# Kernel optimization log

Hardware: AMD Instinct MI355X
Metric: run time of the kernel (lower is better)

Reference implementation:

```python
import jax, jax.numpy as jnp
import numpy as np
import math

D_MODEL = 512
N_HEADS = 8
PATH_LEN = 3
B, L, S = 4, 1024, 1024


def _path_index_structure(L, S, path_length):
    """Precompute the static multi-hop index structure (numpy, trace-time)."""
    i = np.arange(L)[:, None]          # [L,1]
    j = np.arange(S)[None, :]          # [1,S]
    step = (j - i) / path_length       # float
    # Python int() truncates toward zero; i + k*step >= 0 here, so floor == int().
    m1 = np.floor(i + 1 * step).astype(np.int32)  # [L,S] first intermediate point
    m2 = np.floor(i + 2 * step).astype(np.int32)  # [L,S] second intermediate point
    near = np.abs(i - j) <= path_length            # [L,S] bool: direct-score region
    return m1, m2, near


def setup_inputs() -> dict:
    key = jax.random.key(0)
    ks = jax.random.split(key, 7)
    inp = {
        "queries": jax.random.normal(ks[0], (B, L, D_MODEL), dtype=jnp.float32),
        "keys": jax.random.normal(ks[1], (B, S, D_MODEL), dtype=jnp.float32),
        "values": jax.random.normal(ks[2], (B, S, D_MODEL), dtype=jnp.float32),
        # nn.Linear(d_model, d_keys*n_heads, bias=False): stored as [in, out] so y = x @ W
        "W_q": jax.random.normal(ks[3], (D_MODEL, D_MODEL), dtype=jnp.float32) * 0.02,
        "W_k": jax.random.normal(ks[4], (D_MODEL, D_MODEL), dtype=jnp.float32) * 0.02,
        "W_v": jax.random.normal(ks[5], (D_MODEL, D_MODEL), dtype=jnp.float32) * 0.02,
        "W_o": jax.random.normal(ks[6], (D_MODEL, D_MODEL), dtype=jnp.float32) * 0.02,
    }
    return inp


def reference(queries, keys, values, W_q, W_k, W_v, W_o):
    Bv, Lv, _ = queries.shape
    Sv = keys.shape[1]
    H = N_HEADS
    q = (queries @ W_q).reshape(Bv, Lv, H, -1).transpose(0, 2, 1, 3)  # [B,H,L,D]
    k = (keys @ W_k).reshape(Bv, Sv, H, -1).transpose(0, 2, 1, 3)     # [B,H,S,D]
    v = (values @ W_v).reshape(Bv, Sv, H, -1).transpose(0, 2, 1, 3)   # [B,H,S,D]
    D = q.shape[-1]

    scores = jnp.einsum('bhld,bhsd->bhls', q, k) / math.sqrt(D)  # [B,H,L,S]

    # --- path-score modification (vectorized form of the nested loops) ---
    m1, m2, near = _path_index_structure(Lv, Sv, PATH_LEN)
    row = np.arange(Lv)[:, None]
    col = np.arange(Sv)[None, :]
    a = scores[:, :, row, m1]   # scores[:,:,i,m1(i,j)] -> [B,H,L,S]
    b = scores[:, :, m2, col]   # scores[:,:,m2(i,j),j] -> [B,H,L,S]
    # .mean() in the original reduces over BOTH batch and heads to a scalar per (i,j)
    path_mean = jnp.mean(a * b, axis=(0, 1))  # [L,S]
    scores = jnp.where(jnp.asarray(near), scores, path_mean[None, None, :, :])

    attn = jax.nn.softmax(scores, axis=-1)  # dropout p=0 in eval reference
    out = jnp.einsum('bhls,bhsd->blhd', attn, v).reshape(Bv, Lv, H * D)
    out = out @ W_o  # [B,L,d_model]
    return out, attn
```

## Files before the change

### kernel.cpp

```cpp
#include <hip/hip_runtime.h>
#include <math.h>

static constexpr int B_ = 4;
static constexpr int L_ = 1024;
static constexpr int S_ = 1024;
static constexpr int DMODEL = 512;
static constexpr int NH = 8;
static constexpr int DH = 64;
static constexpr int NBH = 32;

typedef __attribute__((ext_vector_type(8))) short s8;
typedef __attribute__((ext_vector_type(4))) float floatx4;

__device__ __forceinline__ short f2bf(float f) {
  unsigned u = __float_as_uint(f);
  return (short)((u + 0x7fffu + ((u >> 16) & 1u)) >> 16);
}
__device__ __forceinline__ float bf2f(short s) {
  return __uint_as_float(((unsigned)(unsigned short)s) << 16);
}

__global__ __launch_bounds__(256)
void cvt_inputs_kernel(const float* __restrict__ q, const float* __restrict__ k,
                       const float* __restrict__ v, short* __restrict__ dst) {
  const int i = blockIdx.x * 256 + threadIdx.x;
  const int arr = i >> 18;
  const int off = (i & 262143) << 3;
  const float* src = (arr == 0) ? q : (arr == 1) ? k : v;
  const float4 f0 = *(const float4*)(src + off);
  const float4 f1 = *(const float4*)(src + off + 4);
  s8 o;
  o[0] = f2bf(f0.x); o[1] = f2bf(f0.y); o[2] = f2bf(f0.z); o[3] = f2bf(f0.w);
  o[4] = f2bf(f1.x); o[5] = f2bf(f1.y); o[6] = f2bf(f1.z); o[7] = f2bf(f1.w);
  *(s8*)(dst + (size_t)arr * 2097152 + off) = o;
}

__global__ __launch_bounds__(256)
void wtrans_kernel(const float* __restrict__ Wq, const float* __restrict__ Wk,
                   const float* __restrict__ Wv, const float* __restrict__ Wo,
                   short* __restrict__ WT) {
  __shared__ float t[32][33];
  const int z = blockIdx.z;
  const float* W = (z == 0) ? Wq : (z == 1) ? Wk : (z == 2) ? Wv : Wo;
  short* dst = WT + (size_t)z * 262144;
  const int k0 = blockIdx.y * 32, n0 = blockIdx.x * 32;
  const int row = threadIdx.x >> 3;
  const int c4 = (threadIdx.x & 7) << 2;
  const float4 f = *(const float4*)(W + (size_t)(k0 + row) * 512 + n0 + c4);
  t[row][c4 + 0] = f.x; t[row][c4 + 1] = f.y; t[row][c4 + 2] = f.z; t[row][c4 + 3] = f.w;
  __syncthreads();
#pragma unroll
  for (int j = 0; j < 4; ++j)
    dst[(size_t)(n0 + row) * 512 + k0 + c4 + j] = f2bf(t[c4 + j][row]);
}

template<int MODE>
__global__ __launch_bounds__(256)
void proj_mfma_kernel(const short* __restrict__ A, const short* __restrict__ WT,
                      void* __restrict__ C, int K) {
  const int tid = threadIdx.x;
  const int lane = tid & 63, w = tid >> 6;
  const int wm = w >> 1, wn = w & 1;
  const int m0 = blockIdx.y * 64, n0 = blockIdx.x * 64;
  const int kl = (lane >> 4) << 3;
  const int rA = m0 + wm * 32 + (lane & 15);
  const int rB = n0 + wn * 32 + (lane & 15);
  const short* pA = A + (size_t)rA * K + kl;
  const short* pB = WT + (size_t)rB * K + kl;
  const size_t f16K = (size_t)16 * K;
  floatx4 acc00 = {0,0,0,0}, acc01 = {0,0,0,0}, acc10 = {0,0,0,0}, acc11 = {0,0,0,0};
  for (int k = 0; k < K; k += 32) {
    const s8 a0 = *(const s8*)(pA + k);
    const s8 a1 = *(const s8*)(pA + f16K + k);
    const s8 b0 = *(const s8*)(pB + k);
    const s8 b1 = *(const s8*)(pB + f16K + k);
    acc00 = __builtin_amdgcn_mfma_f32_16x16x32_bf16(a0, b0, acc00, 0, 0, 0);
    acc01 = __builtin_amdgcn_mfma_f32_16x16x32_bf16(a0, b1, acc01, 0, 0, 0);
    acc10 = __builtin_amdgcn_mfma_f32_16x16x32_bf16(a1, b0, acc10, 0, 0, 0);
    acc11 = __builtin_amdgcn_mfma_f32_16x16x32_bf16(a1, b1, acc11, 0, 0, 0);
  }
  const int crow = (lane >> 4) << 2;
  const int ccol = lane & 15;
#pragma unroll
  for (int fm = 0; fm < 2; ++fm)
#pragma unroll
    for (int fn = 0; fn < 2; ++fn) {
      const floatx4 acc = (fm == 0) ? ((fn == 0) ? acc00 : acc01)
                                    : ((fn == 0) ? acc10 : acc11);
      const int col = n0 + wn * 32 + fn * 16 + ccol;
#pragma unroll
      for (int r = 0; r < 4; ++r) {
        const int row = m0 + wm * 32 + fm * 16 + crow + r;
        if (MODE == 0) {
          const int b = row >> 10, l = row & 1023, h = col >> 6, d = col & 63;
          ((short*)C)[((size_t)((b * NH + h) * L_ + l)) * DH + d] = f2bf(acc[r]);
        } else if (MODE == 1) {
          const int b = row >> 10, s = row & 1023, h = col >> 6, d = col & 63;
          ((short*)C)[((size_t)((b * NH + h) * DH + d)) * S_ + s] = f2bf(acc[r]);
        } else {
          ((float*)C)[(size_t)row * DMODEL + col] = acc[r];
        }
      }
    }
}

__global__ __launch_bounds__(256)
void scores_mfma_kernel(const short* __restrict__ qbf, const short* __restrict__ kbf,
                        float* __restrict__ Sc) {
  const int tid = threadIdx.x;
  const int lane = tid & 63, w = tid >> 6;
  const int wm = w >> 1, wn = w & 1;
  const int m0 = blockIdx.y * 64, n0 = blockIdx.x * 64;
  const int bh = blockIdx.z;
  const int kl = (lane >> 4) << 3;
  const short* pA = qbf + (size_t)bh * L_ * DH + (size_t)(m0 + wm * 32 + (lane & 15)) * DH + kl;
  const short* pB = kbf + (size_t)bh * S_ * DH + (size_t)(n0 + wn * 32 + (lane & 15)) * DH + kl;
  floatx4 acc00 = {0,0,0,0}, acc01 = {0,0,0,0}, acc10 = {0,0,0,0}, acc11 = {0,0,0,0};
#pragma unroll
  for (int k = 0; k < DH; k += 32) {
    const s8 a0 = *(const s8*)(pA + k);
    const s8 a1 = *(const s8*)(pA + 16 * DH + k);
    const s8 b0 = *(const s8*)(pB + k);
    const s8 b1 = *(const s8*)(pB + 16 * DH + k);
    acc00 = __builtin_amdgcn_mfma_f32_16x16x32_bf16(a0, b0, acc00, 0, 0, 0);
    acc01 = __builtin_amdgcn_mfma_f32_16x16x32_bf16(a0, b1, acc01, 0, 0, 0);
    acc10 = __builtin_amdgcn_mfma_f32_16x16x32_bf16(a1, b0, acc10, 0, 0, 0);
    acc11 = __builtin_amdgcn_mfma_f32_16x16x32_bf16(a1, b1, acc11, 0, 0, 0);
  }
  float* Cp = Sc + (size_t)bh * L_ * S_;
  const int crow = (lane >> 4) << 2;
  const int ccol = lane & 15;
#pragma unroll
  for (int fm = 0; fm < 2; ++fm)
#pragma unroll
    for (int fn = 0; fn < 2; ++fn) {
      const floatx4 acc = (fm == 0) ? ((fn == 0) ? acc00 : acc01)
                                    : ((fn == 0) ? acc10 : acc11);
      const int col = n0 + wn * 32 + fn * 16 + ccol;
#pragma unroll
      for (int r = 0; r < 4; ++r) {
        const int row = m0 + wm * 32 + fm * 16 + crow + r;
        Cp[(size_t)row * S_ + col] = acc[r] * 0.125f;
      }
    }
}

__global__ __launch_bounds__(256)
void path_mean_kernel(const float* __restrict__ Sc, float* __restrict__ pm) {
  __shared__ float As[32][36];
  __shared__ float Bs[32][36];
  const int orig = blockIdx.x;
  const int wgid = (orig & 7) * 128 + (orig >> 3);
  const int i0 = (wgid >> 5) << 5;
  const int j0 = (wgid & 31) << 5;
  const int c0 = (2 * i0 + j0) / 3;
  const int c0_al = c0 & ~3;
  const int r0 = (i0 + 2 * j0) / 3;
  const int tid = threadIdx.x;
  const int row_s = tid >> 3;
  const int c4 = tid & 7;
  const int ti = tid >> 3;
  const int tj = tid & 7;
  const int gi = i0 + ti;
  int aoff[4], boff[4];
#pragma unroll
  for (int b = 0; b < 4; ++b) {
    const int gj = j0 + 4 * tj + b;
    const int m1 = (2 * gi + gj) / 3;
    const int m2 = (gi + 2 * gj) / 3;
    aoff[b] = ti * 36 + (m1 - c0_al);
    boff[b] = (m2 - r0) * 36 + (4 * tj + b);
  }
  const int gcA = c0_al + 4 * c4;
  int gcA2 = c0_al + 32; if (gcA2 > 1020) gcA2 = 1020;
  const float* pA  = Sc + (size_t)(i0 + row_s) * S_ + gcA;
  const float* pA2 = Sc + (size_t)(i0 + (tid & 31)) * S_ + gcA2;
  const float* pB  = Sc + (size_t)(r0 + row_s) * S_ + j0 + 4 * c4;
  const float* As0 = &As[0][0];
  const float* Bs0 = &Bs[0][0];
  float acc[4] = {0.f, 0.f, 0.f, 0.f};
  for (int z = 0; z < NBH; ++z) {
    const size_t zo = (size_t)z * (L_ * S_);
    const float4 av = *(const float4*)(pA + zo);
    const float4 bv = *(const float4*)(pB + zo);
    float4 av2;
    if (tid < 32) av2 = *(const float4*)(pA2 + zo);
    __syncthreads();
    *(float4*)&As[row_s][4 * c4] = av;
    if (tid < 32) *(float4*)&As[tid][32] = av2;
    *(float4*)&Bs[row_s][4 * c4] = bv;
    __syncthreads();
#pragma unroll
    for (int b = 0; b < 4; ++b)
      acc[b] = fmaf(As0[aoff[b]], Bs0[boff[b]], acc[b]);
  }
  float4 o = make_float4(acc[0] * (1.f / 32.f), acc[1] * (1.f / 32.f),
                         acc[2] * (1.f / 32.f), acc[3] * (1.f / 32.f));
  *(float4*)&pm[(size_t)gi * S_ + j0 + 4 * tj] = o;
}

__global__ __launch_bounds__(256)
void softmax_kernel(float* __restrict__ Sc, const float* __restrict__ pm) {
  const int r = blockIdx.x;
  const int i = r & 1023;
  float* row = Sc + (size_t)r * S_;
  const float* pmrow = pm + (size_t)i * S_;
  const int tid = threadIdx.x;
  const int j0 = tid << 2;
  const float4 sv = *(const float4*)(row + j0);
  const float4 pv = *(const float4*)(pmrow + j0);
  float vals[4] = {sv.x, sv.y, sv.z, sv.w};
  const float pvals[4] = {pv.x, pv.y, pv.z, pv.w};
  float mx = -1e30f;
#pragma unroll
  for (int u = 0; u < 4; ++u) {
    const int j = j0 + u;
    const int diff = i - j;
    const bool near = (diff <= 3) && (diff >= -3);
    vals[u] = near ? vals[u] : pvals[u];
    mx = fmaxf(mx, vals[u]);
  }
  __shared__ float redm[4];
  __shared__ float reds[4];
  const int lane = tid & 63, wid = tid >> 6;
#pragma unroll
  for (int off = 32; off >= 1; off >>= 1) mx = fmaxf(mx, __shfl_xor(mx, off));
  if (lane == 0) redm[wid] = mx;
  __syncthreads();
  mx = fmaxf(fmaxf(redm[0], redm[1]), fmaxf(redm[2], redm[3]));
  float sum = 0.f;
#pragma unroll
  for (int u = 0; u < 4; ++u) {
    vals[u] = __expf(vals[u] - mx);
    sum += vals[u];
  }
#pragma unroll
  for (int off = 32; off >= 1; off >>= 1) sum += __shfl_xor(sum, off);
  if (lane == 0) reds[wid] = sum;
  __syncthreads();
  sum = reds[0] + reds[1] + reds[2] + reds[3];
  const float inv = 1.f / sum;
  float4 o = make_float4(vals[0] * inv, vals[1] * inv, vals[2] * inv, vals[3] * inv);
  *(float4*)(row + j0) = o;
}

__global__ __launch_bounds__(256)
void pv_mfma_kernel(const float* __restrict__ attn, const short* __restrict__ vT,
                    short* __restrict__ out1) {
  const int tid = threadIdx.x;
  const int lane = tid & 63, w = tid >> 6;
  const int wm = w >> 1, wn = w & 1;
  const int m0 = blockIdx.x * 64;
  const int bh = blockIdx.y;
  const int b = bh >> 3, h = bh & 7;
  const int kl = (lane >> 4) << 3;
  const float* pA = attn + (size_t)bh * L_ * S_ + (size_t)(m0 + wm * 32 + (lane & 15)) * S_ + kl;
  const short* pB = vT + (size_t)bh * DH * S_ + (size_t)(wn * 32 + (lane & 15)) * S_ + kl;
  floatx4 acc00 = {0,0,0,0}, acc01 = {0,0,0,0}, acc10 = {0,0,0,0}, acc11 = {0,0,0,0};
  for (int k = 0; k < S_; k += 32) {
    const float4 fa0 = *(const float4*)(pA + k);
    const float4 fa1 = *(const float4*)(pA + k + 4);
    const float4 fb0 = *(const float4*)(pA + 16 * S_ + k);
    const float4 fb1 = *(const float4*)(pA + 16 * S_ + k + 4);
    s8 a0, a1;
    a0[0] = f2bf(fa0.x); a0[1] = f2bf(fa0.y); a0[2] = f2bf(fa0.z); a0[3] = f2bf(fa0.w);
    a0[4] = f2bf(fa1.x); a0[5] = f2bf(fa1.y); a0[6] = f2bf(fa1.z); a0[7] = f2bf(fa1.w);
    a1[0] = f2bf(fb0.x); a1[1] = f2bf(fb0.y); a1[2] = f2bf(fb0.z); a1[3] = f2bf(fb0.w);
    a1[4] = f2bf(fb1.x); a1[5] = f2bf(fb1.y); a1[6] = f2bf(fb1.z); a1[7] = f2bf(fb1.w);
    const s8 b0 = *(const s8*)(pB + k);
    const s8 b1 = *(const s8*)(pB + 16 * S_ + k);
    acc00 = __builtin_amdgcn_mfma_f32_16x16x32_bf16(a0, b0, acc00, 0, 0, 0);
    acc01 = __builtin_amdgcn_mfma_f32_16x16x32_bf16(a0, b1, acc01, 0, 0, 0);
    acc10 = __builtin_amdgcn_mfma_f32_16x16x32_bf16(a1, b0, acc10, 0, 0, 0);
    acc11 = __builtin_amdgcn_mfma_f32_16x16x32_bf16(a1, b1, acc11, 0, 0, 0);
  }
  const int crow = (lane >> 4) << 2;
  const int ccol = lane & 15;
#pragma unroll
  for (int fm = 0; fm < 2; ++fm)
#pragma unroll
    for (int fn = 0; fn < 2; ++fn) {
      const floatx4 acc = (fm == 0) ? ((fn == 0) ? acc00 : acc01)
                                    : ((fn == 0) ? acc10 : acc11);
      const int d = wn * 32 + fn * 16 + ccol;
#pragma unroll
      for (int r = 0; r < 4; ++r) {
        const int l = m0 + wm * 32 + fm * 16 + crow + r;
        out1[((size_t)(b * L_ + l)) * DMODEL + h * DH + d] = f2bf(acc[r]);
      }
    }
}

extern "C" void kernel_launch(void* const* d_in, const int* in_sizes, int n_in,
                              void* d_out, int out_size, void* d_ws, size_t ws_size,
                              hipStream_t stream) {
  const float* queries = (const float*)d_in[0];
  const float* keys    = (const float*)d_in[1];
  const float* values  = (const float*)d_in[2];
  const float* Wq      = (const float*)d_in[3];
  const float* Wk      = (const float*)d_in[4];
  const float* Wv      = (const float*)d_in[5];
  const float* Wo      = (const float*)d_in[6];

  float* out  = (float*)d_out;
  float* attn = out + (size_t)B_ * L_ * DMODEL;

  char* ws = (char*)d_ws;
  short* xbf  = (short*)(ws);
  short* WT   = (short*)(ws + 12u * 1048576);
  short* qbf  = (short*)(ws + 14u * 1048576);
  short* kbf  = (short*)(ws + 18u * 1048576);
  short* vT   = (short*)(ws + 22u * 1048576);
  float* pm   = (float*)(ws + 26u * 1048576);
  short* out1 = (short*)(ws + 30u * 1048576);

  const dim3 blk(256);

  hipLaunchKernelGGL(cvt_inputs_kernel, dim3(3072), blk, 0, stream,
                     queries, keys, values, xbf);
  hipLaunchKernelGGL(wtrans_kernel, dim3(16, 16, 4), blk, 0, stream,
                     Wq, Wk, Wv, Wo, WT);

  const dim3 gProj(DMODEL / 64, (B_ * L_) / 64);
  hipLaunchKernelGGL((proj_mfma_kernel<0>), gProj, blk, 0, stream,
                     xbf,            WT,               (void*)qbf, DMODEL);
  hipLaunchKernelGGL((proj_mfma_kernel<0>), gProj, blk, 0, stream,
                     xbf + 2097152,  WT + 262144,      (void*)kbf, DMODEL);
  hipLaunchKernelGGL((proj_mfma_kernel<1>), gProj, blk, 0, stream,
                     xbf + 4194304,  WT + 524288,      (void*)vT,  DMODEL);

  const dim3 gSc(S_ / 64, L_ / 64, NBH);
  hipLaunchKernelGGL(scores_mfma_kernel, gSc, blk, 0, stream, qbf, kbf, attn);

  hipLaunchKernelGGL(path_mean_kernel, dim3(1024), blk, 0, stream, attn, pm);

  hipLaunchKernelGGL(softmax_kernel, dim3(NBH * L_), blk, 0, stream, attn, pm);

  hipLaunchKernelGGL(pv_mfma_kernel, dim3(L_ / 64, NBH), blk, 0, stream,
                     attn, vT, out1);

  hipLaunchKernelGGL((proj_mfma_kernel<2>), gProj, blk, 0, stream,
                     out1, WT + 786432, (void*)out, DMODEL);
}
```

Before: 224.6 us.

## Factor softmax into shared path-mean exponentials plus per-row band correction

Outside the near-diagonal band, every (b,h) row takes its values from the same path_mean row. So the softmax is rewritten as a per-row scale c times a shared bf16 exp matrix E, plus a 7-element band correction. The PV GEMM now reads the shared bf16 E instead of converting the fp32 attention for each head, and the band is added in the epilogue using a new row-major V copy. The attention output write still goes through a lighter kernel that also produces the scale and band weights. The cost is an extra V layout, extra small buffers, and bf16 rounding applied before the per-head scale.

```diff
diff --git a/kernel.cpp b/kernel.cpp
--- a/kernel.cpp
+++ b/kernel.cpp
@@ -57,7 +57,7 @@
 template<int MODE>
 __global__ __launch_bounds__(256)
 void proj_mfma_kernel(const short* __restrict__ A, const short* __restrict__ WT,
-                      void* __restrict__ C, int K) {
+                      void* __restrict__ C, short* __restrict__ C2, int K) {
   const int tid = threadIdx.x;
   const int lane = tid & 63, w = tid >> 6;
   const int wm = w >> 1, wn = w & 1;
@@ -94,9 +94,11 @@
         if (MODE == 0) {
           const int b = row >> 10, l = row & 1023, h = col >> 6, d = col & 63;
           ((short*)C)[((size_t)((b * NH + h) * L_ + l)) * DH + d] = f2bf(acc[r]);
-        } else if (MODE == 1) {
+        } else if (MODE == 3) {
           const int b = row >> 10, s = row & 1023, h = col >> 6, d = col & 63;
-          ((short*)C)[((size_t)((b * NH + h) * DH + d)) * S_ + s] = f2bf(acc[r]);
+          const short val = f2bf(acc[r]);
+          ((short*)C)[((size_t)((b * NH + h) * DH + d)) * S_ + s] = val;
+          C2[((size_t)((b * NH + h) * S_ + s)) * DH + d] = val;
         } else {
           ((float*)C)[(size_t)row * DMODEL + col] = acc[r];
         }
@@ -200,53 +202,104 @@
 }
 
 __global__ __launch_bounds__(256)
-void softmax_kernel(float* __restrict__ Sc, const float* __restrict__ pm) {
-  const int r = blockIdx.x;
-  const int i = r & 1023;
-  float* row = Sc + (size_t)r * S_;
-  const float* pmrow = pm + (size_t)i * S_;
-  const int tid = threadIdx.x;
-  const int j0 = tid << 2;
-  const float4 sv = *(const float4*)(row + j0);
-  const float4 pv = *(const float4*)(pmrow + j0);
-  float vals[4] = {sv.x, sv.y, sv.z, sv.w};
-  const float pvals[4] = {pv.x, pv.y, pv.z, pv.w};
+void pm_stats_kernel(const float* __restrict__ pm, short* __restrict__ E,
+                     float* __restrict__ pmmax, float* __restrict__ pmsum) {
+  const int wid = threadIdx.x >> 6, lane = threadIdx.x & 63;
+  const int i = blockIdx.x * 4 + wid;
+  const float* row = pm + (size_t)i * S_;
+  const int j0 = lane << 4;
+  float v[16];
+#pragma unroll
+  for (int c = 0; c < 4; ++c) {
+    const float4 f = *(const float4*)(row + j0 + c * 4);
+    v[c * 4 + 0] = f.x; v[c * 4 + 1] = f.y; v[c * 4 + 2] = f.z; v[c * 4 + 3] = f.w;
+  }
   float mx = -1e30f;
 #pragma unroll
-  for (int u = 0; u < 4; ++u) {
-    const int j = j0 + u;
-    const int diff = i - j;
-    const bool near = (diff <= 3) && (diff >= -3);
-    vals[u] = near ? vals[u] : pvals[u];
-    mx = fmaxf(mx, vals[u]);
-  }
-  __shared__ float redm[4];
-  __shared__ float reds[4];
-  const int lane = tid & 63, wid = tid >> 6;
+  for (int u = 0; u < 16; ++u) {
+    const int d = i - (j0 + u);
+    const bool far = (d > 3) || (d < -3);
+    if (far) mx = fmaxf(mx, v[u]);
+  }
 #pragma unroll
   for (int off = 32; off >= 1; off >>= 1) mx = fmaxf(mx, __shfl_xor(mx, off));
-  if (lane == 0) redm[wid] = mx;
-  __syncthreads();
-  mx = fmaxf(fmaxf(redm[0], redm[1]), fmaxf(redm[2], redm[3]));
   float sum = 0.f;
-#pragma unroll
-  for (int u = 0; u < 4; ++u) {
-    vals[u] = __expf(vals[u] - mx);
-    sum += vals[u];
+  short e[16];
+#pragma unroll
+  for (int u = 0; u < 16; ++u) {
+    const int d = i - (j0 + u);
+    const bool far = (d > 3) || (d < -3);
+    const float ev = far ? __expf(v[u] - mx) : 0.f;
+    sum += ev;
+    e[u] = f2bf(ev);
   }
 #pragma unroll
   for (int off = 32; off >= 1; off >>= 1) sum += __shfl_xor(sum, off);
-  if (lane == 0) reds[wid] = sum;
-  __syncthreads();
-  sum = reds[0] + reds[1] + reds[2] + reds[3];
-  const float inv = 1.f / sum;
-  float4 o = make_float4(vals[0] * inv, vals[1] * inv, vals[2] * inv, vals[3] * inv);
-  *(float4*)(row + j0) = o;
-}
-
-__global__ __launch_bounds__(256)
-void pv_mfma_kernel(const float* __restrict__ attn, const short* __restrict__ vT,
-                    short* __restrict__ out1) {
+  s8 o0, o1;
+#pragma unroll
+  for (int u = 0; u < 8; ++u) { o0[u] = e[u]; o1[u] = e[8 + u]; }
+  short* Erow = E + (size_t)i * S_ + j0;
+  *(s8*)Erow = o0;
+  *(s8*)(Erow + 8) = o1;
+  if (lane == 0) { pmmax[i] = mx; pmsum[i] = sum; }
+}
+
+__global__ __launch_bounds__(256)
+void attn_write_kernel(float* __restrict__ Sc, const short* __restrict__ E,
+                       const float* __restrict__ pmmax, const float* __restrict__ pmsum,
+                       float* __restrict__ cvec, float* __restrict__ band) {
+  const int wid = threadIdx.x >> 6, lane = threadIdx.x & 63;
+  const int i = blockIdx.x * 4 + wid;
+  const int bh = blockIdx.y;
+  float* row = Sc + ((size_t)bh * L_ + i) * S_;
+
+  const int j_u = i - 3 + lane;
+  float s_u = -1e30f;
+  if (lane < 7 && j_u >= 0 && j_u < S_) s_u = row[j_u];
+
+  float bm = s_u;
+#pragma unroll
+  for (int off = 32; off >= 1; off >>= 1) bm = fmaxf(bm, __shfl_xor(bm, off));
+  const float pmx = pmmax[i];
+  const float m = fmaxf(pmx, bm);
+  const float bexp = __expf(s_u - m);
+  float bsum = bexp;
+#pragma unroll
+  for (int off = 32; off >= 1; off >>= 1) bsum += __shfl_xor(bsum, off);
+  const float cpm = __expf(pmx - m);
+  const float inv = 1.f / (bsum + pmsum[i] * cpm);
+  const float c = cpm * inv;
+
+  if (lane == 0) cvec[bh * L_ + i] = c;
+  if (lane < 8) band[((size_t)(bh * L_ + i)) << 3 | lane] = __expf(s_u - m) * inv;
+
+  const short* Erow = E + (size_t)i * S_;
+  const int j0 = lane << 4;
+  const s8 e0 = *(const s8*)(Erow + j0);
+  const s8 e1 = *(const s8*)(Erow + j0 + 8);
+  float outv[16];
+#pragma unroll
+  for (int u = 0; u < 8; ++u) {
+    outv[u]     = bf2f(e0[u]) * c;
+    outv[8 + u] = bf2f(e1[u]) * c;
+  }
+#pragma unroll
+  for (int t = 0; t < 16; ++t) {
+    const int j = j0 + t;
+    const int d = j - i;
+    if (d >= -3 && d <= 3)
+      outv[t] = __expf(row[j] - m) * inv;
+  }
+#pragma unroll
+  for (int c4 = 0; c4 < 4; ++c4)
+    *(float4*)(row + j0 + c4 * 4) =
+        make_float4(outv[c4 * 4], outv[c4 * 4 + 1], outv[c4 * 4 + 2], outv[c4 * 4 + 3]);
+}
+
+__global__ __launch_bounds__(256)
+void ev_kernel(const short* __restrict__ E, const short* __restrict__ vT,
+               const short* __restrict__ vS, const float* __restrict__ cvec,
+               const float* __restrict__ band, short* __restrict__ out1) {
   const int tid = threadIdx.x;
   const int lane = tid & 63, w = tid >> 6;
   const int wm = w >> 1, wn = w & 1;
@@ -254,19 +307,12 @@
   const int bh = blockIdx.y;
   const int b = bh >> 3, h = bh & 7;
   const int kl = (lane >> 4) << 3;
-  const float* pA = attn + (size_t)bh * L_ * S_ + (size_t)(m0 + wm * 32 + (lane & 15)) * S_ + kl;
+  const short* pA = E + (size_t)(m0 + wm * 32 + (lane & 15)) * S_ + kl;
   const short* pB = vT + (size_t)bh * DH * S_ + (size_t)(wn * 32 + (lane & 15)) * S_ + kl;
   floatx4 acc00 = {0,0,0,0}, acc01 = {0,0,0,0}, acc10 = {0,0,0,0}, acc11 = {0,0,0,0};
   for (int k = 0; k < S_; k += 32) {
-    const float4 fa0 = *(const float4*)(pA + k);
-    const float4 fa1 = *(const float4*)(pA + k + 4);
-    const float4 fb0 = *(const float4*)(pA + 16 * S_ + k);
-    const float4 fb1 = *(const float4*)(pA + 16 * S_ + k + 4);
-    s8 a0, a1;
-    a0[0] = f2bf(fa0.x); a0[1] = f2bf(fa0.y); a0[2] = f2bf(fa0.z); a0[3] = f2bf(fa0.w);
-    a0[4] = f2bf(fa1.x); a0[5] = f2bf(fa1.y); a0[6] = f2bf(fa1.z); a0[7] = f2bf(fa1.w);
-    a1[0] = f2bf(fb0.x); a1[1] = f2bf(fb0.y); a1[2] = f2bf(fb0.z); a1[3] = f2bf(fb0.w);
-    a1[4] = f2bf(fb1.x); a1[5] = f2bf(fb1.y); a1[6] = f2bf(fb1.z); a1[7] = f2bf(fb1.w);
+    const s8 a0 = *(const s8*)(pA + k);
+    const s8 a1 = *(const s8*)(pA + 16 * S_ + k);
     const s8 b0 = *(const s8*)(pB + k);
     const s8 b1 = *(const s8*)(pB + 16 * S_ + k);
     acc00 = __builtin_amdgcn_mfma_f32_16x16x32_bf16(a0, b0, acc00, 0, 0, 0);
@@ -279,14 +325,27 @@
 #pragma unroll
   for (int fm = 0; fm < 2; ++fm)
 #pragma unroll
-    for (int fn = 0; fn < 2; ++fn) {
-      const floatx4 acc = (fm == 0) ? ((fn == 0) ? acc00 : acc01)
-                                    : ((fn == 0) ? acc10 : acc11);
-      const int d = wn * 32 + fn * 16 + ccol;
-#pragma unroll
-      for (int r = 0; r < 4; ++r) {
-        const int l = m0 + wm * 32 + fm * 16 + crow + r;
-        out1[((size_t)(b * L_ + l)) * DMODEL + h * DH + d] = f2bf(acc[r]);
+    for (int r = 0; r < 4; ++r) {
+      const int l = m0 + wm * 32 + fm * 16 + crow + r;
+      const float c = cvec[bh * L_ + l];
+      const float* bap = band + (((size_t)(bh * L_ + l)) << 3);
+      const float4 b0v = *(const float4*)bap;
+      const float4 b1v = *(const float4*)(bap + 4);
+      const float bav[7] = {b0v.x, b0v.y, b0v.z, b0v.w, b1v.x, b1v.y, b1v.z};
+#pragma unroll
+      for (int fn = 0; fn < 2; ++fn) {
+        const floatx4 acc = (fm == 0) ? ((fn == 0) ? acc00 : acc01)
+                                      : ((fn == 0) ? acc10 : acc11);
+        const int d = wn * 32 + fn * 16 + ccol;
+        float corr = 0.f;
+#pragma unroll
+        for (int u = 0; u < 7; ++u) {
+          int j = l - 3 + u;
+          const int jc = j < 0 ? 0 : (j > 1023 ? 1023 : j);
+          corr = fmaf(bav[u], bf2f(vS[((size_t)bh * S_ + jc) * DH + d]), corr);
+        }
+        const float val = fmaf(c, acc[r], corr);
+        out1[((size_t)(b * L_ + l)) * DMODEL + h * DH + d] = f2bf(val);
       }
     }
 }
@@ -311,8 +370,14 @@
   short* qbf  = (short*)(ws + 14u * 1048576);
   short* kbf  = (short*)(ws + 18u * 1048576);
   short* vT   = (short*)(ws + 22u * 1048576);
-  float* pm   = (float*)(ws + 26u * 1048576);
-  short* out1 = (short*)(ws + 30u * 1048576);
+  short* vS   = (short*)(ws + 26u * 1048576);
+  float* pm   = (float*)(ws + 30u * 1048576);
+  short* E    = (short*)(ws + 34u * 1048576);
+  float* pmmax= (float*)(ws + 36u * 1048576);
+  float* pmsum= (float*)(ws + 36u * 1048576 + 4096);
+  float* cvec = (float*)(ws + 36u * 1048576 + 65536);
+  float* band = (float*)(ws + 37u * 1048576);
+  short* out1 = (short*)(ws + 38u * 1048576);
 
   const dim3 blk(256);
 
@@ -323,22 +388,26 @@
 
   const dim3 gProj(DMODEL / 64, (B_ * L_) / 64);
   hipLaunchKernelGGL((proj_mfma_kernel<0>), gProj, blk, 0, stream,
-                     xbf,            WT,               (void*)qbf, DMODEL);
+                     xbf,           WT,          (void*)qbf, (short*)nullptr, DMODEL);
   hipLaunchKernelGGL((proj_mfma_kernel<0>), gProj, blk, 0, stream,
-                     xbf + 2097152,  WT + 262144,      (void*)kbf, DMODEL);
-  hipLaunchKernelGGL((proj_mfma_kernel<1>), gProj, blk, 0, stream,
-                     xbf + 4194304,  WT + 524288,      (void*)vT,  DMODEL);
+                     xbf + 2097152, WT + 262144, (void*)kbf, (short*)nullptr, DMODEL);
+  hipLaunchKernelGGL((proj_mfma_kernel<3>), gProj, blk, 0, stream,
+                     xbf + 4194304, WT + 524288, (void*)vT,  vS,              DMODEL);
 
   const dim3 gSc(S_ / 64, L_ / 64, NBH);
   hipLaunchKernelGGL(scores_mfma_kernel, gSc, blk, 0, stream, qbf, kbf, attn);
 
   hipLaunchKernelGGL(path_mean_kernel, dim3(1024), blk, 0, stream, attn, pm);
 
-  hipLaunchKernelGGL(softmax_kernel, dim3(NBH * L_), blk, 0, stream, attn, pm);
-
-  hipLaunchKernelGGL(pv_mfma_kernel, dim3(L_ / 64, NBH), blk, 0, stream,
-                     attn, vT, out1);
+  hipLaunchKernelGGL(pm_stats_kernel, dim3(L_ / 4), blk, 0, stream,
+                     pm, E, pmmax, pmsum);
+
+  hipLaunchKernelGGL(attn_write_kernel, dim3(L_ / 4, NBH), blk, 0, stream,
+                     attn, E, pmmax, pmsum, cvec, band);
+
+  hipLaunchKernelGGL(ev_kernel, dim3(L_ / 64, NBH), blk, 0, stream,
+                     E, vT, vS, cvec, band, out1);
 
   hipLaunchKernelGGL((proj_mfma_kernel<2>), gProj, blk, 0, stream,
-                     out1, WT + 786432, (void*)out, DMODEL);
-}
+                     out1, WT + 786432, (void*)out, (short*)nullptr, DMODEL);
+}
```

New measurement: 225.6 us. About the same (+0.5%).
